# Kernel optimization log

Measured on AMD Instinct MI355X. Metric: run time of the kernel, lower is better.

## Reference

```python
import jax, jax.numpy as jnp
import numpy as np

D_MODEL, D_STATE, B, S = 1024, 64, 8, 2048


def setup_inputs() -> dict:
    key = jax.random.key(0)
    ks = jax.random.split(key, 14)
    inp = {"x": jax.random.normal(ks[0], (B, S, D_MODEL), jnp.float32)}
    names = ["cog", "beh", "env", "delta", "Bp", "Cp"]
    for i, n in enumerate(names):
        inp[f"W_{n}"] = jax.random.normal(ks[1 + 2 * i], (D_STATE, D_MODEL), jnp.float32) / np.sqrt(D_MODEL)
        inp[f"b_{n}"] = jnp.zeros((D_STATE,), jnp.float32)
    # torch init is log(|randn|+1e-4); we use strictly-negative A_log so the
    # length-2048 multiplicative recurrence stays finite (A_log is a learned
    # parameter, so its value is free; the math of forward is unchanged).
    inp["A_log"] = -jnp.abs(jax.random.normal(ks[13], (D_STATE, D_STATE), jnp.float32)) - 0.1
    return inp


def reference(x, W_cog, b_cog, W_beh, b_beh, W_env, b_env,
              W_delta, b_delta, W_Bp, b_Bp, W_Cp, b_Cp, A_log):
    # gating terms (computed in the source but never used downstream)
    A_t = (jax.nn.sigmoid(x @ W_cog.T + b_cog)
           * jax.nn.sigmoid(x @ W_beh.T + b_beh)
           * jax.nn.sigmoid(x @ W_env.T + b_env))
    del A_t

    delta = jax.nn.softplus(x @ W_delta.T + b_delta)   # [B,S,N]
    Bt = x @ W_Bp.T + b_Bp                             # [B,S,N]
    Ct = x @ W_Cp.T + b_Cp                             # [B,S,N]
    u = Bt * x[:, :, :D_STATE]                         # [B,S,N]

    # Faithful to torch broadcasting: after step 0 the carried state h is
    # [B,N,N] with h[b,i,j] = exp(A_log[i,j]*delta[b,t,i]) * h_prev[b,i,j] + u[b,t,j]
    def step(h, td):
        d, u_t, c_t = td                               # each [B,N]
        A = jnp.exp(A_log[None, :, :] * d[:, :, None]) # [B,N,N]
        h = A * h + u_t[:, None, :]
        y = jnp.einsum('bj,bij->bi', c_t, h)           # [B,N]
        return h, y

    h0 = jnp.zeros((x.shape[0], D_STATE, D_STATE), x.dtype)
    _, ys = jax.lax.scan(
        step, h0,
        (delta.transpose(1, 0, 2), u.transpose(1, 0, 2), Ct.transpose(1, 0, 2)))
    # torch stacks y_t of shape [B,1,N] along dim=1 -> [B,S,1,N]
    return ys.transpose(1, 0, 2)[:, :, None, :]
```

## Files before the change

kernel.cpp:

```cpp
#include <hip/hip_runtime.h>
#include <math.h>

#define DM   1024
#define DS   64
#define BATCH 8
#define SEQ  2048
#define CL   32
#define NC   64

typedef __bf16 bf16x8 __attribute__((ext_vector_type(8)));
typedef float  f32x4  __attribute__((ext_vector_type(4)));

#if __has_builtin(__builtin_amdgcn_exp2f)
#define EXP2(v) __builtin_amdgcn_exp2f(v)
#else
#define EXP2(v) __expf(0.69314718056f * (v))
#endif

__global__ __launch_bounds__(256) void wconv_kernel(
    const float* __restrict__ Wd, const float* __restrict__ Wb,
    const float* __restrict__ Wc, __bf16* __restrict__ Wp)
{
    int idx = blockIdx.x * 256 + threadIdx.x;
    int k  = idx & 1023;
    int n  = idx >> 10;
    const float* W = (n < 64) ? Wd : (n < 128 ? Wb : Wc);
    float v = W[(size_t)(n & 63) * DM + k];
    int kt = k >> 5, kk = k & 31;
    Wp[((size_t)kt * 192 + n) * 32 + kk] = (__bf16)v;
}

__global__ __launch_bounds__(256, 2) void projp1_full(
    const float* __restrict__ x, const __bf16* __restrict__ Wp,
    const float* __restrict__ bd, const float* __restrict__ bb,
    const float* __restrict__ bc, const float* __restrict__ A_log,
    float* __restrict__ delta_g, float* __restrict__ u_g,
    float* __restrict__ ct_g,
    float* __restrict__ E, float* __restrict__ Dsum)
{
    __shared__ __bf16 sB[2][12288];
    __shared__ __bf16 sA[2][32 * 72];
    __shared__ float  s_d[CL * 64];
    __shared__ float  s_u[CL * 64];

    const int tid  = threadIdx.x;
    const int row0 = blockIdx.x * 32;

    const int lane = tid & 63, wv = tid >> 6;
    const int l15  = lane & 15, quad = lane >> 4;
    const int nbase = wv * 48;

    const int am = tid >> 3;
    const int ak = tid & 7;
    const float* xga = x + (size_t)(row0 + am) * DM + ak * 8;

    f32x4 acc[2][3];
    #pragma unroll
    for (int mt = 0; mt < 2; ++mt)
        #pragma unroll
        for (int nt = 0; nt < 3; ++nt)
            acc[mt][nt] = (f32x4){0.f, 0.f, 0.f, 0.f};

    float4 areg[2];

#if __has_builtin(__builtin_amdgcn_global_load_lds)
    #define LOADB(kb, bi) do {                                                \
        _Pragma("unroll")                                                     \
        for (int it = 0; it < 6; ++it) {                                      \
            const __bf16* gsrc =                                              \
                Wp + (size_t)(kb) * 12288 + (tid + it * 256) * 8;             \
            __bf16* ldst = &sB[bi][(tid + it * 256) * 8];                     \
            __builtin_amdgcn_global_load_lds(                                 \
                (const __attribute__((address_space(1))) void*)gsrc,          \
                (__attribute__((address_space(3))) void*)ldst, 16, 0, 0);     \
        }                                                                     \
    } while (0)
#else
    #define LOADB(kb, bi) do {                                                \
        _Pragma("unroll")                                                     \
        for (int it = 0; it < 6; ++it) {                                      \
            uint4 t = *(const uint4*)(                                        \
                Wp + (size_t)(kb) * 12288 + (tid + it * 256) * 8);            \
            *(uint4*)&sB[bi][(tid + it * 256) * 8] = t;                       \
        }                                                                     \
    } while (0)
#endif
    #define LOADA(kb) do {                                                    \
        areg[0] = *(const float4*)(xga + (kb) * 64);                          \
        areg[1] = *(const float4*)(xga + (kb) * 64 + 4);                      \
    } while (0)
    #define STAGEA(bi) do {                                                   \
        bf16x8 hv = {(__bf16)areg[0].x, (__bf16)areg[0].y,                    \
                     (__bf16)areg[0].z, (__bf16)areg[0].w,                    \
                     (__bf16)areg[1].x, (__bf16)areg[1].y,                    \
                     (__bf16)areg[1].z, (__bf16)areg[1].w};                   \
        *(bf16x8*)&sA[bi][am * 72 + ak * 8] = hv;                             \
    } while (0)
    #define COMPUTE(bi) do {                                                  \
        _Pragma("unroll")                                                     \
        for (int s = 0; s < 2; ++s) {                                         \
            bf16x8 af[2];                                                     \
            _Pragma("unroll")                                                 \
            for (int mt = 0; mt < 2; ++mt)                                    \
                af[mt] = *(const bf16x8*)                                     \
                    &sA[bi][(mt * 16 + l15) * 72 + s * 32 + quad * 8];        \
            _Pragma("unroll")                                                 \
            for (int nt = 0; nt < 3; ++nt) {                                  \
                bf16x8 bv = *(const bf16x8*)                                  \
                    &sB[bi][s * 6144 + (nbase + nt * 16 + l15) * 32           \
                            + quad * 8];                                      \
                _Pragma("unroll")                                             \
                for (int mt = 0; mt < 2; ++mt)                                \
                    acc[mt][nt] = __builtin_amdgcn_mfma_f32_16x16x32_bf16(    \
                        af[mt], bv, acc[mt][nt], 0, 0, 0);                    \
            }                                                                 \
        }                                                                     \
    } while (0)

    LOADB(0, 0);
    LOADA(0);
    STAGEA(0);
    __syncthreads();

    int buf = 0;
    for (int kb = 0; kb < 16; ++kb) {
        if (kb < 15) {
            LOADB(kb + 1, buf ^ 1);
            LOADA(kb + 1);
        }
        COMPUTE(buf);
        if (kb < 15) STAGEA(buf ^ 1);
        __syncthreads();
        buf ^= 1;
    }
    #undef LOADB
    #undef LOADA
    #undef STAGEA
    #undef COMPUTE

    #pragma unroll
    for (int nt = 0; nt < 3; ++nt) {
        int gn  = nbase + nt * 16 + l15;
        int mat = (nbase + nt * 16) >> 6;
        int col = gn & 63;
        float bias = (mat == 0) ? bd[col] : (mat == 1 ? bb[col] : bc[col]);
        #pragma unroll
        for (int mt = 0; mt < 2; ++mt) {
            #pragma unroll
            for (int r = 0; r < 4; ++r) {
                int tl = mt * 16 + quad * 4 + r;
                int m  = row0 + tl;
                float v = acc[mt][nt][r] + bias;
                if (mat == 0) {
                    float sp = (v > 20.f) ? v : __logf(1.f + __expf(v));
                    delta_g[(size_t)m * DS + col] = sp;
                    s_d[tl * 64 + col] = sp;
                } else if (mat == 1) {
                    float uu = v * x[(size_t)m * DM + col];
                    u_g[(size_t)m * DS + col] = uu;
                    s_u[tl * 64 + col] = uu;
                } else {
                    ct_g[(size_t)m * DS + col] = v;
                }
            }
        }
    }
    __syncthreads();

    const int bidx = row0 >> 11;
    const int cidx = (row0 >> 5) & 63;
    const int si = tid & 63;
    const int sj = tid >> 6;

    float alog[16];
    {
        const float4* ar = (const float4*)(A_log + si * 64 + sj * 16);
        #pragma unroll
        for (int qq = 0; qq < 4; ++qq) {
            float4 v = ar[qq];
            alog[4*qq+0] = v.x * 1.44269504f; alog[4*qq+1] = v.y * 1.44269504f;
            alog[4*qq+2] = v.z * 1.44269504f; alog[4*qq+3] = v.w * 1.44269504f;
        }
    }

    float h[16];
    #pragma unroll
    for (int k = 0; k < 16; ++k) h[k] = 0.f;
    float dsum = 0.f;

    for (int t = 0; t < CL; ++t) {
        float d = s_d[t * 64 + si];
        dsum += d;
        const float* up = s_u + t * 64 + sj * 16;
        #pragma unroll
        for (int k = 0; k < 16; ++k)
            h[k] = EXP2(alog[k] * d) * h[k] + up[k];
    }

    float* eo = E + (((size_t)cidx * BATCH + bidx) * 64 + si) * 64 + sj * 16;
    #pragma unroll
    for (int qq = 0; qq < 4; ++qq)
        ((float4*)eo)[qq] = make_float4(h[4*qq], h[4*qq+1], h[4*qq+2], h[4*qq+3]);
    if (sj == 0) Dsum[((size_t)cidx * BATCH + bidx) * 64 + si] = dsum;
}

__global__ __launch_bounds__(256) void pass23_kernel(
    const float* __restrict__ delta_g, const float* __restrict__ u_g,
    const float* __restrict__ ct_g, const float* __restrict__ A_log,
    const float* __restrict__ E, const float* __restrict__ Dsum,
    float* __restrict__ out)
{
    __shared__ float s_d[CL * 64];
    __shared__ float s_u[CL * 64];
    __shared__ float s_c[CL * 64];

    const int c = blockIdx.x, b = blockIdx.y, tid = threadIdx.x;
    const int t0 = c * CL;

    const float4* dg = (const float4*)(delta_g + ((size_t)b * SEQ + t0) * DS);
    const float4* ug = (const float4*)(u_g     + ((size_t)b * SEQ + t0) * DS);
    const float4* cg = (const float4*)(ct_g    + ((size_t)b * SEQ + t0) * DS);
    #pragma unroll
    for (int it = 0; it < (CL * 64 / 4) / 256; ++it) {
        int f = tid + it * 256;
        ((float4*)s_d)[f] = dg[f];
        ((float4*)s_u)[f] = ug[f];
        ((float4*)s_c)[f] = cg[f];
    }

    const int i  = tid >> 2;
    const int jg = tid & 3;

    float alog[16];
    {
        const float4* ar = (const float4*)(A_log + i * 64 + jg * 16);
        #pragma unroll
        for (int qq = 0; qq < 4; ++qq) {
            float4 v = ar[qq];
            alog[4*qq+0] = v.x * 1.44269504f; alog[4*qq+1] = v.y * 1.44269504f;
            alog[4*qq+2] = v.z * 1.44269504f; alog[4*qq+3] = v.w * 1.44269504f;
        }
    }

    float h[16];
    #pragma unroll
    for (int k = 0; k < 16; ++k) h[k] = 0.f;

    for (int cp = 0; cp < c; ++cp) {
        float ds = Dsum[((size_t)cp * BATCH + b) * 64 + i];
        const float4* ep = (const float4*)(
            E + (((size_t)cp * BATCH + b) * 64 + i) * 64 + jg * 16);
        float4 e0 = ep[0], e1 = ep[1], e2 = ep[2], e3 = ep[3];
        float ev[16] = {e0.x,e0.y,e0.z,e0.w, e1.x,e1.y,e1.z,e1.w,
                        e2.x,e2.y,e2.z,e2.w, e3.x,e3.y,e3.z,e3.w};
        #pragma unroll
        for (int k = 0; k < 16; ++k)
            h[k] = EXP2(alog[k] * ds) * h[k] + ev[k];
    }
    __syncthreads();

    for (int t = 0; t < CL; ++t) {
        float d = s_d[t * 64 + i];
        const float* up  = s_u + t * 64 + jg * 16;
        const float* cp2 = s_c + t * 64 + jg * 16;
        float part = 0.f;
        #pragma unroll
        for (int k = 0; k < 16; ++k) {
            h[k] = EXP2(alog[k] * d) * h[k] + up[k];
            part += cp2[k] * h[k];
        }
        part += __shfl_xor(part, 1);
        part += __shfl_xor(part, 2);
        if (jg == 0)
            out[((size_t)b * SEQ + t0 + t) * DS + i] = part;
    }
}

extern "C" void kernel_launch(void* const* d_in, const int* in_sizes, int n_in,
                              void* d_out, int out_size, void* d_ws, size_t ws_size,
                              hipStream_t stream)
{
    const float* x     = (const float*)d_in[0];
    const float* Wd    = (const float*)d_in[7];
    const float* bd    = (const float*)d_in[8];
    const float* Wb    = (const float*)d_in[9];
    const float* bb    = (const float*)d_in[10];
    const float* Wc    = (const float*)d_in[11];
    const float* bc    = (const float*)d_in[12];
    const float* A_log = (const float*)d_in[13];
    float* out = (float*)d_out;

    float* ws = (float*)d_ws;
    float* delta_g = ws;
    float* u_g     = ws + 1 * 1048576;
    float* ct_g    = ws + 2 * 1048576;
    float* E       = ws + 3 * 1048576;
    float* Dsum    = ws + 5 * 1048576;
    __bf16* Wp     = (__bf16*)(ws + 5 * 1048576 + 65536);

    wconv_kernel<<<768, 256, 0, stream>>>(Wd, Wb, Wc, Wp);
    projp1_full<<<512, 256, 0, stream>>>(
        x, Wp, bd, bb, bc, A_log, delta_g, u_g, ct_g, E, Dsum);
    pass23_kernel<<<dim3(NC, BATCH), 256, 0, stream>>>(
        delta_g, u_g, ct_g, A_log, E, Dsum, out);
}
```

Measured before the change: 187.3 us.

## Add hierarchical group-level chunk state combine to shorten prefix scan

Adds a kernel that combines chunk end-states in groups of eight, producing group carry states and summed decay exponents. The main scan kernel then needs at most seven group steps plus seven chunk steps instead of up to sixty-three serial chunk steps, and it prefetches the next chunk's state while computing the current one. This costs an extra launch, extra workspace, and a small low-occupancy kernel.

```diff
diff --git a/kernel.cpp b/kernel.cpp
--- a/kernel.cpp
+++ b/kernel.cpp
@@ -204,10 +204,79 @@
     if (sj == 0) Dsum[((size_t)cidx * BATCH + bidx) * 64 + si] = dsum;
 }
 
+__device__ __forceinline__ void scan_range(
+    const float* __restrict__ Eb, const float* __restrict__ Db,
+    int n0, int n1, int bb_, int i_, int jg_,
+    const float* __restrict__ alog, float* __restrict__ h)
+{
+    if (n0 >= n1) return;
+    size_t idx = ((size_t)n0 * BATCH + bb_) * 64 + i_;
+    float dsA = Db[idx];
+    const float4* ep = (const float4*)(Eb + idx * 64 + jg_ * 16);
+    float4 e0 = ep[0], e1 = ep[1], e2 = ep[2], e3 = ep[3];
+    for (int n = n0; n < n1; ++n) {
+        float dsN = 0.f;
+        float4 f0 = make_float4(0.f,0.f,0.f,0.f), f1 = f0, f2 = f0, f3 = f0;
+        if (n + 1 < n1) {
+            size_t idx2 = ((size_t)(n + 1) * BATCH + bb_) * 64 + i_;
+            dsN = Db[idx2];
+            const float4* fp = (const float4*)(Eb + idx2 * 64 + jg_ * 16);
+            f0 = fp[0]; f1 = fp[1]; f2 = fp[2]; f3 = fp[3];
+        }
+        float ev[16] = {e0.x,e0.y,e0.z,e0.w, e1.x,e1.y,e1.z,e1.w,
+                        e2.x,e2.y,e2.z,e2.w, e3.x,e3.y,e3.z,e3.w};
+        #pragma unroll
+        for (int k = 0; k < 16; ++k)
+            h[k] = EXP2(alog[k] * dsA) * h[k] + ev[k];
+        dsA = dsN; e0 = f0; e1 = f1; e2 = f2; e3 = f3;
+    }
+}
+
+__global__ __launch_bounds__(256) void group_kernel(
+    const float* __restrict__ E, const float* __restrict__ Dsum,
+    const float* __restrict__ A_log,
+    float* __restrict__ Eg, float* __restrict__ Dg)
+{
+    const int g2 = blockIdx.x >> 3, b2 = blockIdx.x & 7;
+    const int tid = threadIdx.x;
+    const int i  = tid >> 2;
+    const int jg = tid & 3;
+
+    float alog[16];
+    {
+        const float4* ar = (const float4*)(A_log + i * 64 + jg * 16);
+        #pragma unroll
+        for (int qq = 0; qq < 4; ++qq) {
+            float4 v = ar[qq];
+            alog[4*qq+0] = v.x * 1.44269504f; alog[4*qq+1] = v.y * 1.44269504f;
+            alog[4*qq+2] = v.z * 1.44269504f; alog[4*qq+3] = v.w * 1.44269504f;
+        }
+    }
+
+    float hg[16];
+    #pragma unroll
+    for (int k = 0; k < 16; ++k) hg[k] = 0.f;
+    scan_range(E, Dsum, g2 * 8, g2 * 8 + 8, b2, i, jg, alog, hg);
+
+    float4* ego = (float4*)(Eg + (((size_t)g2 * BATCH + b2) * 64 + i) * 64 + jg * 16);
+    ego[0] = make_float4(hg[0],  hg[1],  hg[2],  hg[3]);
+    ego[1] = make_float4(hg[4],  hg[5],  hg[6],  hg[7]);
+    ego[2] = make_float4(hg[8],  hg[9],  hg[10], hg[11]);
+    ego[3] = make_float4(hg[12], hg[13], hg[14], hg[15]);
+    if (jg == 0) {
+        float Dacc = 0.f;
+        #pragma unroll
+        for (int q = 0; q < 8; ++q)
+            Dacc += Dsum[((size_t)(g2 * 8 + q) * BATCH + b2) * 64 + i];
+        Dg[((size_t)g2 * BATCH + b2) * 64 + i] = Dacc;
+    }
+}
+
 __global__ __launch_bounds__(256) void pass23_kernel(
     const float* __restrict__ delta_g, const float* __restrict__ u_g,
     const float* __restrict__ ct_g, const float* __restrict__ A_log,
     const float* __restrict__ E, const float* __restrict__ Dsum,
+    const float* __restrict__ Eg, const float* __restrict__ Dg,
     float* __restrict__ out)
 {
     __shared__ float s_d[CL * 64];
@@ -245,18 +314,9 @@
     float h[16];
     #pragma unroll
     for (int k = 0; k < 16; ++k) h[k] = 0.f;
-
-    for (int cp = 0; cp < c; ++cp) {
-        float ds = Dsum[((size_t)cp * BATCH + b) * 64 + i];
-        const float4* ep = (const float4*)(
-            E + (((size_t)cp * BATCH + b) * 64 + i) * 64 + jg * 16);
-        float4 e0 = ep[0], e1 = ep[1], e2 = ep[2], e3 = ep[3];
-        float ev[16] = {e0.x,e0.y,e0.z,e0.w, e1.x,e1.y,e1.z,e1.w,
-                        e2.x,e2.y,e2.z,e2.w, e3.x,e3.y,e3.z,e3.w};
-        #pragma unroll
-        for (int k = 0; k < 16; ++k)
-            h[k] = EXP2(alog[k] * ds) * h[k] + ev[k];
-    }
+    const int g = c >> 3;
+    scan_range(Eg, Dg, 0, g, b, i, jg, alog, h);
+    scan_range(E, Dsum, g * 8, c, b, i, jg, alog, h);
     __syncthreads();
 
     for (int t = 0; t < CL; ++t) {
@@ -280,6 +340,7 @@
                               void* d_out, int out_size, void* d_ws, size_t ws_size,
                               hipStream_t stream)
 {
+    (void)in_sizes; (void)n_in; (void)out_size; (void)ws_size;
     const float* x     = (const float*)d_in[0];
     const float* Wd    = (const float*)d_in[7];
     const float* bd    = (const float*)d_in[8];
@@ -295,12 +356,15 @@
     float* u_g     = ws + 1 * 1048576;
     float* ct_g    = ws + 2 * 1048576;
     float* E       = ws + 3 * 1048576;
-    float* Dsum    = ws + 5 * 1048576;
-    __bf16* Wp     = (__bf16*)(ws + 5 * 1048576 + 65536);
+    float* Dsum    = ws + 5242880;
+    float* Eg      = ws + 5275648;
+    float* Dg      = ws + 5537792;
+    __bf16* Wp     = (__bf16*)(ws + 5541888);
 
     wconv_kernel<<<768, 256, 0, stream>>>(Wd, Wb, Wc, Wp);
     projp1_full<<<512, 256, 0, stream>>>(
         x, Wp, bd, bb, bc, A_log, delta_g, u_g, ct_g, E, Dsum);
+    group_kernel<<<64, 256, 0, stream>>>(E, Dsum, A_log, Eg, Dg);
     pass23_kernel<<<dim3(NC, BATCH), 256, 0, stream>>>(
-        delta_g, u_g, ct_g, A_log, E, Dsum, out);
-}
+        delta_g, u_g, ct_g, A_log, E, Dsum, Eg, Dg, out);
+}
```

New measurement: 174.7 us. 1.07x faster.
